# Optimization experiments

Hardware: AMD Instinct MI355X
Metric: run time of the kernel (lower is better)

## Reference

```python
import jax, jax.numpy as jnp
import numpy as np

# ---- constants from the source module ----
N_SAMPLES = 2 ** 15          # exp.n_samples
N_FRAMES = 128
N_HARMONICS = 8
N_EVENTS = 8
FILT_SIZE = 16               # freq_domain_filter_size
N_NOTES = 128                # len(scale)
NYQ = 22050.0 / 2.0          # samplerate nyquist
MIN_F0 = 40.0 / NYQ
F0_SPAN = (3000.0 / NYQ) - MIN_F0
MIN_RES = 0.5
RES_SPAN = 1.0 - MIN_RES
B_EVENTS = 128               # batch(16) * n_events(8)

# packed layout (build_param_slices order):
SL_F0 = slice(0, N_NOTES)                       # 0:128
SL_AMP = slice(N_NOTES + N_FRAMES, N_NOTES + 2 * N_FRAMES)   # 256:384
SL_HAMP = slice(N_NOTES + 2 * N_FRAMES, N_NOTES + 2 * N_FRAMES + N_HARMONICS)  # 384:392
SL_HDEC = slice(N_NOTES + 2 * N_FRAMES + N_HARMONICS, N_NOTES + 2 * N_FRAMES + 2 * N_HARMONICS)  # 392:400
SL_FENV = slice(N_NOTES + 2 * N_FRAMES + 2 * N_HARMONICS, N_NOTES + 2 * N_FRAMES + 2 * N_HARMONICS + FILT_SIZE)  # 400:416


def interp_linear(x, out_size):
    """F.interpolate(..., mode='linear', align_corners=False) on last dim of [B,C,L]."""
    L = x.shape[-1]
    scale = L / out_size
    coords = (jnp.arange(out_size, dtype=x.dtype) + 0.5) * scale - 0.5
    coords = jnp.clip(coords, 0.0, L - 1)
    i0 = jnp.floor(coords).astype(jnp.int32)
    i1 = jnp.minimum(i0 + 1, L - 1)
    w = coords - i0.astype(x.dtype)
    return x[..., i0] * (1.0 - w) + x[..., i1] * w


def setup_inputs() -> dict:
    key = jax.random.key(0)
    k1, k2 = jax.random.split(key)
    packed = jax.random.uniform(k1, (B_EVENTS, N_NOTES + 2 * N_FRAMES + 2 * N_HARMONICS + FILT_SIZE), dtype=jnp.float32)
    # musical-scale center frequencies, normalized by nyquist (geometric 20..3000 Hz)
    hz = 20.0 * (3000.0 / 20.0) ** (np.arange(N_NOTES) / (N_NOTES - 1))
    frequencies = jnp.asarray(hz / NYQ, dtype=jnp.float32)
    global_amp = jnp.full((1,), 5000.0, dtype=jnp.float32)
    osc_amp = jnp.full((1,), 50.0, dtype=jnp.float32)
    noise = jax.random.uniform(k2, (B_EVENTS, 1, N_SAMPLES), dtype=jnp.float32, minval=-1.0, maxval=1.0)
    return {"packed": packed, "frequencies": frequencies, "global_amp": global_amp,
            "osc_amp": osc_amp, "noise": noise}


def reference(packed, frequencies, global_amp, osc_amp, noise):
    B = packed.shape[0]
    # ---- f0 (discrete): softmax over notes, expectation, squared, repeated per frame ----
    f0_scalar = jax.nn.softmax(packed[:, SL_F0], axis=-1) @ frequencies          # [B]
    f0 = (f0_scalar ** 2)[:, None, None] * jnp.ones((1, 1, N_FRAMES), packed.dtype)  # [B,1,F]
    f0 = f0 * NYQ
    f0 = MIN_F0 + f0 * F0_SPAN
    # (the torch line `f0 + f0 + f0_fine` has no assignment -> no effect; f0_fine unused)

    # ---- oscillator bank ----
    harm_factors = jnp.arange(1, N_HARMONICS + 1, dtype=packed.dtype)
    osc = f0 * harm_factors[None, :, None]                      # [B,H,F]
    radians = osc / NYQ * jnp.pi
    radians = jnp.where(radians >= jnp.pi, 0.0, radians)
    radians = interp_linear(radians, N_SAMPLES)                  # [B,H,S]
    osc_bank = jnp.sin(jnp.cumsum(radians, axis=-1)) * osc_amp   # [B,H,S]

    # ---- per-harmonic amplitude recurrence (scan over frames) ----
    harm_decay = MIN_RES + packed[:, SL_HDEC] * RES_SPAN         # [B,H]
    harm_amp = packed[:, SL_HAMP]                                # [B,H]
    amp = packed[:, SL_AMP][:, None, :] * 2.0 - 1.0              # [B,1,F]

    def step(current, amp_i):                                    # current [B,H], amp_i [B,1]
        cur = jnp.maximum(current + amp_i * harm_amp, 0.0)       # clamp(0, inf)
        return cur * harm_decay, cur

    amp_frames = jnp.moveaxis(amp[:, 0, :], 1, 0)[:, :, None]    # [F,B,1]
    _, res = jax.lax.scan(step, jnp.zeros((B, N_HARMONICS), packed.dtype), amp_frames)
    res = jnp.moveaxis(res, 0, 2)                                # [B,H,F]
    res_full = interp_linear(res, N_SAMPLES)                     # [B,H,S]

    # ---- FFT-filtered noise ----
    amp_full = interp_linear(amp, N_SAMPLES)                     # [B,1,S]
    nf = packed[:, SL_FENV][:, None, :]                          # [B,1,16]
    nf = interp_linear(nf, N_SAMPLES // 2)
    nf = jnp.pad(nf, ((0, 0), (0, 0), (0, 1)))                   # [B,1,S//2+1]
    noise_scaled = noise * global_amp
    spec = jnp.fft.rfft(noise_scaled, axis=-1, norm='ortho')
    filt = spec * nf
    noise_out = jnp.fft.irfft(filt, n=N_SAMPLES, axis=-1, norm='ortho')
    noise_out = noise_out * jnp.where(amp_full >= 0, amp_full, 0.2 * amp_full)  # leaky_relu(0.2)

    # ---- combine ----
    x = res_full * osc_bank                                      # [B,H,S]
    x = noise_out / N_HARMONICS + x                              # broadcast [B,1,S]
    x = x.reshape(-1, N_EVENTS, N_HARMONICS, N_SAMPLES)
    x = jnp.sum(x, axis=(1, 2)).reshape(-1, 1, N_SAMPLES)        # [batch,1,S]
    return x
```

## Files before the change

### kernel.cpp

```cpp
#include <hip/hip_runtime.h>
#include <math.h>

#define PCK_STRIDE 416
#define N_SAMPLES  32768
#define FFT_M      16384
#define B_EVENTS   128
#define N_GROUPS   16
#define NT         1024
#define PI_F 3.14159265358979323846f
#define RT2H 0.70710678118654752f

#define MAP(i) ((i) + (((i) >> 5) << 2))
#define LDS_N  18432

__device__ inline float filt_at(const float* __restrict__ f, int k) {
    if (k >= FFT_M) return 0.0f;
    float c = ((float)k + 0.5f) * (1.0f / 1024.0f) - 0.5f;
    c = fminf(fmaxf(c, 0.0f), 15.0f);
    int i0 = (int)floorf(c);
    int i1 = min(i0 + 1, 15);
    float w = c - (float)i0;
    return f[i0] * (1.0f - w) + f[i1] * w;
}

template<int L>
__device__ inline void r4_dif_stage(float* re, float* im, int tid) {
    constexpr int q = L >> 2;
    constexpr float ang = -6.28318530717958647692f / (float)L;
    #pragma unroll 1
    for (int s = 0; s < (FFT_M / 4) / NT; ++s) {
        int m = tid + s * NT;
        int t = m & (q - 1);
        int i0 = ((m & ~(q - 1)) << 2) | t;
        int ia = MAP(i0), ib = MAP(i0 + q), ic = MAP(i0 + 2 * q), id = MAP(i0 + 3 * q);
        float ar = re[ia], ai = im[ia];
        float br = re[ib], bi = im[ib];
        float cr = re[ic], ci = im[ic];
        float dr = re[id], di = im[id];
        float s1, c1; __sincosf(ang * (float)t, &s1, &c1);
        float c2 = c1 * c1 - s1 * s1, s2 = 2.0f * c1 * s1;
        float c3 = c2 * c1 - s2 * s1, s3 = c2 * s1 + s2 * c1;
        float s0r = ar + cr, s0i = ai + ci;
        float t1r = br + dr, t1i = bi + di;
        float d0r = ar - cr, d0i = ai - ci;
        float d1r = br - dr, d1i = bi - di;
        re[ia] = s0r + t1r; im[ia] = s0i + t1i;
        float er = s0r - t1r, ei = s0i - t1i;
        re[ib] = er * c2 - ei * s2; im[ib] = er * s2 + ei * c2;
        float fr = d0r + d1i, fi = d0i - d1r;
        re[ic] = fr * c1 - fi * s1; im[ic] = fr * s1 + fi * c1;
        float gr = d0r - d1i, gi = d0i + d1r;
        re[id] = gr * c3 - gi * s3; im[id] = gr * s3 + gi * c3;
    }
    __syncthreads();
}

template<int L>
__device__ inline void r4_dit_stage(float* re, float* im, int tid) {
    constexpr int q = L >> 2;
    constexpr float ang = 6.28318530717958647692f / (float)L;
    #pragma unroll 1
    for (int s = 0; s < (FFT_M / 4) / NT; ++s) {
        int m = tid + s * NT;
        int t = m & (q - 1);
        int i0 = ((m & ~(q - 1)) << 2) | t;
        int ia = MAP(i0), ib = MAP(i0 + q), ic = MAP(i0 + 2 * q), id = MAP(i0 + 3 * q);
        float ar = re[ia], ai = im[ia];
        float br = re[ib], bi = im[ib];
        float cr = re[ic], ci = im[ic];
        float dr = re[id], di = im[id];
        float s1, c1; __sincosf(ang * (float)t, &s1, &c1);
        float c2 = c1 * c1 - s1 * s1, s2 = 2.0f * c1 * s1;
        float tbr = br * c2 - bi * s2, tbi = br * s2 + bi * c2;
        float tdr = dr * c2 - di * s2, tdi = dr * s2 + di * c2;
        float B0r = ar + tbr, B0i = ai + tbi;
        float B1r = ar - tbr, B1i = ai - tbi;
        float B2r = cr + tdr, B2i = ci + tdi;
        float B3r = cr - tdr, B3i = ci - tdi;
        float t0r = B2r * c1 - B2i * s1, t0i = B2r * s1 + B2i * c1;
        float t1r = -B3r * s1 - B3i * c1, t1i = B3r * c1 - B3i * s1;
        re[ia] = B0r + t0r; im[ia] = B0i + t0i;
        re[ib] = B1r + t1r; im[ib] = B1i + t1i;
        re[ic] = B0r - t0r; im[ic] = B0i - t0i;
        re[id] = B1r - t1r; im[id] = B1i - t1i;
    }
    __syncthreads();
}

__global__ __launch_bounds__(NT)
void fft_filter_kernel(
    const float* __restrict__ noise, const float* __restrict__ packed,
    const float* __restrict__ gamp, float* __restrict__ noise_out,
    const float* __restrict__ freqs, float* __restrict__ rW, float* __restrict__ res)
{
    extern __shared__ float smem[];
    float* re = smem;
    float* im = smem + LDS_N;
    float* filt = smem + 2 * LDS_N;
    const int b = blockIdx.x;
    const int tid = threadIdx.x;
    const float g = gamp[0];

    const float2* nz = (const float2*)(noise + (size_t)b * N_SAMPLES);
    #pragma unroll 1
    for (int s = 0; s < 8192 / NT; ++s) {
        int j = tid + s * NT;
        float2 v0 = nz[j];
        float2 v1 = nz[j + 8192];
        float ur = v0.x * g, ui = v0.y * g;
        float wr = v1.x * g, wi = v1.y * g;
        float s1, c1; __sincosf((-PI_F / 8192.0f) * (float)j, &s1, &c1);
        int a0 = MAP(j), a1 = MAP(j + 8192);
        re[a0] = ur + wr; im[a0] = ui + wi;
        float dr = ur - wr, di = ui - wi;
        re[a1] = dr * c1 - di * s1;
        im[a1] = dr * s1 + di * c1;
    }
    if (tid >= 64 && tid < 80) filt[tid - 64] = packed[b * PCK_STRIDE + 400 + (tid - 64)];

    if (tid < 64) {
        const float* row = packed + b * PCK_STRIDE;
        float n0 = row[tid], n1 = row[tid + 64];
        float fq0 = freqs[tid], fq1 = freqs[tid + 64];
        float mx = fmaxf(n0, n1);
        #pragma unroll
        for (int off = 32; off >= 1; off >>= 1) mx = fmaxf(mx, __shfl_xor(mx, off));
        float e0 = __expf(n0 - mx), e1 = __expf(n1 - mx);
        float den = e0 + e1, num = e0 * fq0 + e1 * fq1;
        #pragma unroll
        for (int off = 32; off >= 1; off >>= 1) {
            den += __shfl_xor(den, off);
            num += __shfl_xor(num, off);
        }
        float ampA = row[256 + tid] * 2.0f - 1.0f;
        float ampB = row[320 + tid] * 2.0f - 1.0f;
        int h = tid & 7;
        float ha = row[384 + h];
        float hd = 0.5f + row[392 + h] * 0.5f;
        const float MIN_F0 = 40.0f / 11025.0f;
        const float F0_SPAN = 3000.0f / 11025.0f - 40.0f / 11025.0f;
        float f0s = num / den;
        float f0 = MIN_F0 + f0s * f0s * 11025.0f * F0_SPAN;
        float r = f0 * (float)(h + 1) * (PI_F / 11025.0f);
        if (r >= PI_F) r = 0.0f;
        if (tid < 8) rW[b * 8 + tid] = r;
        float cur = 0.0f;
        float* rr = res + (b * 8 + h) * 128;
        for (int f = 0; f < 64; ++f) {
            float av = __shfl(ampA, f);
            float c = fmaxf(cur + av * ha, 0.0f);
            if (tid < 8) rr[f] = c;
            cur = c * hd;
        }
        for (int f = 0; f < 64; ++f) {
            float av = __shfl(ampB, f);
            float c = fmaxf(cur + av * ha, 0.0f);
            if (tid < 8) rr[64 + f] = c;
            cur = c * hd;
        }
    }
    __syncthreads();

    r4_dif_stage<8192>(re, im, tid);
    r4_dif_stage<2048>(re, im, tid);
    r4_dif_stage<512>(re, im, tid);
    r4_dif_stage<128>(re, im, tid);
    r4_dif_stage<32>(re, im, tid);

    #pragma unroll 1
    for (int s = 0; s < 2048 / NT; ++s) {
        int m = (2048 / NT) * tid + s;
        int a = MAP(8 * m);
        float4 r0 = *(const float4*)(re + a);
        float4 r1 = *(const float4*)(re + a + 4);
        float4 q0 = *(const float4*)(im + a);
        float4 q1 = *(const float4*)(im + a + 4);
        float t0r = r0.x + r1.x, t0i = q0.x + q1.x;
        float u0r = r0.x - r1.x, u0i = q0.x - q1.x;
        float d1r = r0.y - r1.y, d1i = q0.y - q1.y;
        float t1r = r0.y + r1.y, t1i = q0.y + q1.y;
        float u1r = RT2H * (d1r + d1i), u1i = RT2H * (d1i - d1r);
        float t2r = r0.z + r1.z, t2i = q0.z + q1.z;
        float d2r = r0.z - r1.z, d2i = q0.z - q1.z;
        float u2r = d2i, u2i = -d2r;
        float t3r = r0.w + r1.w, t3i = q0.w + q1.w;
        float d3r = r0.w - r1.w, d3i = q0.w - q1.w;
        float u3r = RT2H * (d3i - d3r), u3i = -RT2H * (d3r + d3i);
        float A0r = t0r + t2r, A0i = t0i + t2i;
        float A2r = t0r - t2r, A2i = t0i - t2i;
        float A1r = t1r + t3r, A1i = t1i + t3i;
        float e3r = t1r - t3r, e3i = t1i - t3i;
        float A3r = e3i, A3i = -e3r;
        float B0r = u0r + u2r, B0i = u0i + u2i;
        float B2r = u0r - u2r, B2i = u0i - u2i;
        float B1r = u1r + u3r, B1i = u1i + u3i;
        float f3r = u1r - u3r, f3i = u1i - u3i;
        float B3r = f3i, B3i = -f3r;
        r0.x = A0r + A1r; q0.x = A0i + A1i;
        r0.y = A0r - A1r; q0.y = A0i - A1i;
        r0.z = A2r + A3r; q0.z = A2i + A3i;
        r0.w = A2r - A3r; q0.w = A2i - A3i;
        r1.x = B0r + B1r; q1.x = B0i + B1i;
        r1.y = B0r - B1r; q1.y = B0i - B1i;
        r1.z = B2r + B3r; q1.z = B2i + B3i;
        r1.w = B2r - B3r; q1.w = B2i - B3i;
        *(float4*)(re + a) = r0; *(float4*)(re + a + 4) = r1;
        *(float4*)(im + a) = q0; *(float4*)(im + a + 4) = q1;
    }
    __syncthreads();

    const float invM = 1.0f / (float)FFT_M;
    #pragma unroll 1
    for (int s = 0; s < 8192 / NT; ++s) {
        int jj = (tid + s * NT) << 1;
        if (jj == 0) {
            int p0 = MAP(0);
            float z0r = re[p0], z0i = im[p0];
            float y = 0.5f * filt_at(filt, 0) * (z0r + z0i) * invM;
            re[p0] = y; im[p0] = y;
            int p1 = MAP(1);
            float H = filt_at(filt, 8192) * invM;
            re[p1] *= H; im[p1] *= H;
        } else {
            int k = (int)(__brev((unsigned)jj) >> 18);
            int kq = FFT_M - k;
            int pk = MAP(jj);
            int pq = MAP((int)(__brev((unsigned)kq) >> 18));
            float zkr = re[pk], zki = im[pk];
            float zqr = re[pq], zqi = im[pq];
            float Er = 0.5f * (zkr + zqr), Ei = 0.5f * (zki - zqi);
            float Or = 0.5f * (zki + zqi), Oi = 0.5f * (zqr - zkr);
            float th = (float)k * (PI_F / (float)FFT_M);
            float s1, c1; __sincosf(th, &s1, &c1);
            float ts = -s1;
            float tOr = c1 * Or - ts * Oi;
            float tOi = c1 * Oi + ts * Or;
            float Hk = filt_at(filt, k);
            float Hq = filt_at(filt, kq);
            float Ykr = Hk * (Er + tOr), Yki = Hk * (Ei + tOi);
            float Cr  = Hq * (Er - tOr), Ci  = Hq * (Ei - tOi);
            float Ar = 0.5f * (Ykr + Cr), Ai = 0.5f * (Yki + Ci);
            float Br = 0.5f * (Ykr - Cr), Bi = 0.5f * (Yki - Ci);
            re[pk] = (Ar + ts * Br - c1 * Bi) * invM;
            im[pk] = (Ai + c1 * Br + ts * Bi) * invM;
            re[pq] = (Ar + c1 * Bi - ts * Br) * invM;
            im[pq] = (-Ai + c1 * Br + ts * Bi) * invM;
        }
    }
    __syncthreads();

    #pragma unroll 1
    for (int s = 0; s < 2048 / NT; ++s) {
        int m = (2048 / NT) * tid + s;
        int a = MAP(8 * m);
        float4 r0 = *(const float4*)(re + a);
        float4 r1 = *(const float4*)(re + a + 4);
        float4 q0 = *(const float4*)(im + a);
        float4 q1 = *(const float4*)(im + a + 4);
        float A0r = r0.x + r0.y, A0i = q0.x + q0.y;
        float A1r = r0.x - r0.y, A1i = q0.x - q0.y;
        float A2r = r0.z + r0.w, A2i = q0.z + q0.w;
        float A3r = r0.z - r0.w, A3i = q0.z - q0.w;
        float B0r = r1.x + r1.y, B0i = q1.x + q1.y;
        float B1r = r1.x - r1.y, B1i = q1.x - q1.y;
        float B2r = r1.z + r1.w, B2i = q1.z + q1.w;
        float B3r = r1.z - r1.w, B3i = q1.z - q1.w;
        float t0r = A0r + A2r, t0i = A0i + A2i;
        float t2r = A0r - A2r, t2i = A0i - A2i;
        float w3r = -A3i, w3i = A3r;
        float t1r = A1r + w3r, t1i = A1i + w3i;
        float t3r = A1r - w3r, t3i = A1i - w3i;
        float u0r = B0r + B2r, u0i = B0i + B2i;
        float u2r = B0r - B2r, u2i = B0i - B2i;
        float x3r = -B3i, x3i = B3r;
        float u1r = B1r + x3r, u1i = B1i + x3i;
        float u3r = B1r - x3r, u3i = B1i - x3i;
        float w1r = RT2H * (u1r - u1i), w1i = RT2H * (u1r + u1i);
        float w2r = -u2i,               w2i = u2r;
        float w5r = RT2H * (-u3r - u3i), w5i = RT2H * (u3r - u3i);
        r0.x = t0r + u0r; q0.x = t0i + u0i;
        r1.x = t0r - u0r; q1.x = t0i - u0i;
        r0.y = t1r + w1r; q0.y = t1i + w1i;
        r1.y = t1r - w1r; q1.y = t1i - w1i;
        r0.z = t2r + w2r; q0.z = t2i + w2i;
        r1.z = t2r - w2r; q1.z = t2i - w2i;
        r0.w = t3r + w5r; q0.w = t3i + w5i;
        r1.w = t3r - w5r; q1.w = t3i - w5i;
        *(float4*)(re + a) = r0; *(float4*)(re + a + 4) = r1;
        *(float4*)(im + a) = q0; *(float4*)(im + a + 4) = q1;
    }
    __syncthreads();

    r4_dit_stage<32>(re, im, tid);
    r4_dit_stage<128>(re, im, tid);
    r4_dit_stage<512>(re, im, tid);
    r4_dit_stage<2048>(re, im, tid);
    r4_dit_stage<8192>(re, im, tid);

    float2* oz = (float2*)(noise_out + (size_t)b * N_SAMPLES);
    #pragma unroll 1
    for (int s = 0; s < 8192 / NT; ++s) {
        int j = tid + s * NT;
        int a0 = MAP(j), a1 = MAP(j + 8192);
        float ur = re[a0], ui = im[a0];
        float xr = re[a1], xi = im[a1];
        float s1, c1; __sincosf((PI_F / 8192.0f) * (float)j, &s1, &c1);
        float wr = xr * c1 - xi * s1, wi = xr * s1 + xi * c1;
        oz[j] = make_float2(ur + wr, ui + wi);
        oz[j + 8192] = make_float2(ur - wr, ui - wi);
    }
}

__global__ __launch_bounds__(256) void assemble_kernel(
    const float* __restrict__ packed, const float* __restrict__ rW,
    const float* __restrict__ res, const float* __restrict__ noise_out,
    const float* __restrict__ oamp, float* __restrict__ out)
{
    const int g = blockIdx.y;
    const int chunk = blockIdx.x;
    const int tid = threadIdx.x;
    const int n = chunk * 256 + tid;
    const int fb = chunk - 1;

    __shared__ float s_res[8][8][3];
    __shared__ float s_ampf[8][3];
    __shared__ float s_r[8][8];
    if (tid < 192) {
        int e = tid / 24, rem = tid % 24, h = rem / 3, j = rem % 3;
        int f = min(max(fb + j, 0), 127);
        s_res[e][h][j] = res[((g * 8 + e) * 8 + h) * 128 + f];
    }
    if (tid < 24) {
        int e = tid / 3, j = tid % 3;
        int f = min(max(fb + j, 0), 127);
        s_ampf[e][j] = packed[(g * 8 + e) * PCK_STRIDE + 256 + f] * 2.0f - 1.0f;
    }
    if (tid >= 192 && tid < 256) {
        int u = tid - 192;
        s_r[u / 8][u % 8] = rW[g * 64 + u];
    }
    __syncthreads();

    float coords = ((float)n + 0.5f) * (1.0f / 256.0f) - 0.5f;
    coords = fminf(fmaxf(coords, 0.0f), 127.0f);
    int i0 = (int)floorf(coords);
    float w = coords - (float)i0;
    int j0 = i0 - fb;
    float osc50 = oamp[0];
    float pn = (float)(n + 1);
    float wm = 1.0f - w;

    float acc = 0.0f;
    #pragma unroll
    for (int e = 0; e < 8; ++e) {
        int b = g * 8 + e;
        float nv = noise_out[(size_t)b * N_SAMPLES + n];
        float av = s_ampf[e][j0] * wm + s_ampf[e][j0 + 1] * w;
        float gate = (av >= 0.0f) ? av : 0.2f * av;
        acc += nv * gate;
        float sn, cn; __sincosf(pn * s_r[e][0], &sn, &cn);
        float c2 = 2.0f * cn;
        float shm1 = 0.0f, sh = sn;
        #pragma unroll
        for (int h = 0; h < 8; ++h) {
            float rsv = s_res[e][h][j0] * wm + s_res[e][h][j0 + 1] * w;
            float sv = (s_r[e][h] != 0.0f) ? sh : 0.0f;
            acc += rsv * osc50 * sv;
            float nx = c2 * sh - shm1;
            shm1 = sh; sh = nx;
        }
    }
    out[(size_t)g * N_SAMPLES + n] = acc;
}

extern "C" void kernel_launch(void* const* d_in, const int* in_sizes, int n_in,
                              void* d_out, int out_size, void* d_ws, size_t ws_size,
                              hipStream_t stream) {
    const float* packed = (const float*)d_in[0];
    const float* freqs  = (const float*)d_in[1];
    const float* gamp   = (const float*)d_in[2];
    const float* oamp   = (const float*)d_in[3];
    const float* noise  = (const float*)d_in[4];
    float* out = (float*)d_out;

    float* ws = (float*)d_ws;
    float* noise_out = ws;
    float* res = ws + (size_t)B_EVENTS * N_SAMPLES;
    float* rW  = res + B_EVENTS * 8 * 128;

    fft_filter_kernel<<<B_EVENTS, NT, (2 * LDS_N + 16) * sizeof(float), stream>>>(
        noise, packed, gamp, noise_out, freqs, rW, res);
    assemble_kernel<<<dim3(N_SAMPLES / 256, N_GROUPS), 256, 0, stream>>>(
        packed, rW, res, noise_out, oamp, out);
}
```

Baseline: 117.8 us.

## Fuse assembly into FFT kernel with atomic accumulation into output

Removes the separate assemble kernel and the global noise_out/res/rW round trip. After the inverse FFT, each block applies the amplitude gate, synthesizes the harmonic oscillator sum from LDS-resident resonance and amp tables, and atomically adds its per-sample contribution into the group output, which is zeroed with a memset first. Each thread now processes 16 contiguous samples with an incremental sin/cos rotation. This adds 8-way atomic contention per output element, uncoalesced strided atomics, and rotation-accumulated rounding error, and it leaves only 128 blocks to do all of the work.

```diff
diff --git a/kernel.cpp b/kernel.cpp
--- a/kernel.cpp
+++ b/kernel.cpp
@@ -5,13 +5,13 @@
 #define N_SAMPLES  32768
 #define FFT_M      16384
 #define B_EVENTS   128
-#define N_GROUPS   16
 #define NT         1024
 #define PI_F 3.14159265358979323846f
 #define RT2H 0.70710678118654752f
 
 #define MAP(i) ((i) + (((i) >> 5) << 2))
 #define LDS_N  18432
+#define LDS_TOTAL (2 * LDS_N + 16 + 1024 + 128 + 8)
 
 __device__ inline float filt_at(const float* __restrict__ f, int k) {
     if (k >= FFT_M) return 0.0f;
@@ -90,13 +90,16 @@
 __global__ __launch_bounds__(NT)
 void fft_filter_kernel(
     const float* __restrict__ noise, const float* __restrict__ packed,
-    const float* __restrict__ gamp, float* __restrict__ noise_out,
-    const float* __restrict__ freqs, float* __restrict__ rW, float* __restrict__ res)
+    const float* __restrict__ gamp, const float* __restrict__ oamp,
+    const float* __restrict__ freqs, float* __restrict__ out)
 {
     extern __shared__ float smem[];
     float* re = smem;
     float* im = smem + LDS_N;
-    float* filt = smem + 2 * LDS_N;
+    float* filt   = smem + 2 * LDS_N;
+    float* s_resd = filt + 16;
+    float* s_amp  = s_resd + 1024;
+    float* s_rw   = s_amp + 128;
     const int b = blockIdx.x;
     const int tid = threadIdx.x;
     const float g = gamp[0];
@@ -134,6 +137,8 @@
         }
         float ampA = row[256 + tid] * 2.0f - 1.0f;
         float ampB = row[320 + tid] * 2.0f - 1.0f;
+        s_amp[tid] = ampA;
+        s_amp[64 + tid] = ampB;
         int h = tid & 7;
         float ha = row[384 + h];
         float hd = 0.5f + row[392 + h] * 0.5f;
@@ -142,20 +147,23 @@
         float f0s = num / den;
         float f0 = MIN_F0 + f0s * f0s * 11025.0f * F0_SPAN;
         float r = f0 * (float)(h + 1) * (PI_F / 11025.0f);
-        if (r >= PI_F) r = 0.0f;
-        if (tid < 8) rW[b * 8 + tid] = r;
+        float m = 1.0f;
+        if (r >= PI_F) { r = 0.0f; m = 0.0f; }
+        float scale = m * oamp[0];
+        if (tid < 8) s_rw[tid] = r;
         float cur = 0.0f;
-        float* rr = res + (b * 8 + h) * 128;
+        #pragma unroll 1
         for (int f = 0; f < 64; ++f) {
             float av = __shfl(ampA, f);
             float c = fmaxf(cur + av * ha, 0.0f);
-            if (tid < 8) rr[f] = c;
+            if (tid < 8) s_resd[h * 128 + f] = c * scale;
             cur = c * hd;
         }
+        #pragma unroll 1
         for (int f = 0; f < 64; ++f) {
             float av = __shfl(ampB, f);
             float c = fmaxf(cur + av * ha, 0.0f);
-            if (tid < 8) rr[64 + f] = c;
+            if (tid < 8) s_resd[h * 128 + 64 + f] = c * scale;
             cur = c * hd;
         }
     }
@@ -297,80 +305,65 @@
     r4_dit_stage<2048>(re, im, tid);
     r4_dit_stage<8192>(re, im, tid);
 
-    float2* oz = (float2*)(noise_out + (size_t)b * N_SAMPLES);
-    #pragma unroll 1
-    for (int s = 0; s < 8192 / NT; ++s) {
-        int j = tid + s * NT;
-        int a0 = MAP(j), a1 = MAP(j + 8192);
-        float ur = re[a0], ui = im[a0];
-        float xr = re[a1], xi = im[a1];
-        float s1, c1; __sincosf((PI_F / 8192.0f) * (float)j, &s1, &c1);
-        float wr = xr * c1 - xi * s1, wi = xr * s1 + xi * c1;
-        oz[j] = make_float2(ur + wr, ui + wi);
-        oz[j + 8192] = make_float2(ur - wr, ui - wi);
-    }
-}
-
-__global__ __launch_bounds__(256) void assemble_kernel(
-    const float* __restrict__ packed, const float* __restrict__ rW,
-    const float* __restrict__ res, const float* __restrict__ noise_out,
-    const float* __restrict__ oamp, float* __restrict__ out)
-{
-    const int g = blockIdx.y;
-    const int chunk = blockIdx.x;
-    const int tid = threadIdx.x;
-    const int n = chunk * 256 + tid;
-    const int fb = chunk - 1;
-
-    __shared__ float s_res[8][8][3];
-    __shared__ float s_ampf[8][3];
-    __shared__ float s_r[8][8];
-    if (tid < 192) {
-        int e = tid / 24, rem = tid % 24, h = rem / 3, j = rem % 3;
-        int f = min(max(fb + j, 0), 127);
-        s_res[e][h][j] = res[((g * 8 + e) * 8 + h) * 128 + f];
-    }
-    if (tid < 24) {
-        int e = tid / 3, j = tid % 3;
-        int f = min(max(fb + j, 0), 127);
-        s_ampf[e][j] = packed[(g * 8 + e) * PCK_STRIDE + 256 + f] * 2.0f - 1.0f;
-    }
-    if (tid >= 192 && tid < 256) {
-        int u = tid - 192;
-        s_r[u / 8][u % 8] = rW[g * 64 + u];
-    }
-    __syncthreads();
-
-    float coords = ((float)n + 0.5f) * (1.0f / 256.0f) - 0.5f;
-    coords = fminf(fmaxf(coords, 0.0f), 127.0f);
-    int i0 = (int)floorf(coords);
-    float w = coords - (float)i0;
-    int j0 = i0 - fb;
-    float osc50 = oamp[0];
-    float pn = (float)(n + 1);
-    float wm = 1.0f - w;
-
-    float acc = 0.0f;
-    #pragma unroll
-    for (int e = 0; e < 8; ++e) {
-        int b = g * 8 + e;
-        float nv = noise_out[(size_t)b * N_SAMPLES + n];
-        float av = s_ampf[e][j0] * wm + s_ampf[e][j0 + 1] * w;
-        float gate = (av >= 0.0f) ? av : 0.2f * av;
-        acc += nv * gate;
-        float sn, cn; __sincosf(pn * s_r[e][0], &sn, &cn);
-        float c2 = 2.0f * cn;
-        float shm1 = 0.0f, sh = sn;
-        #pragma unroll
-        for (int h = 0; h < 8; ++h) {
-            float rsv = s_res[e][h][j0] * wm + s_res[e][h][j0 + 1] * w;
-            float sv = (s_r[e][h] != 0.0f) ? sh : 0.0f;
-            acc += rsv * osc50 * sv;
-            float nx = c2 * sh - shm1;
-            shm1 = sh; sh = nx;
-        }
-    }
-    out[(size_t)g * N_SAMPLES + n] = acc;
+    {
+        float* outg = out + (size_t)(b >> 3) * N_SAMPLES;
+        const float r1v = s_rw[0];
+        float rs, rc; __sincosf(r1v, &rs, &rc);
+        #pragma unroll 1
+        for (int run = 0; run < 2; ++run) {
+            const int tbase = 16 * tid + run * 16384;
+            float sn, cn; __sincosf((float)(tbase + 1) * r1v, &sn, &cn);
+            int cur = -1;
+            float Ah[8], Bh[8];
+            float aA = 0.0f, aB = 0.0f;
+            #pragma unroll 1
+            for (int s = 0; s < 8; ++s) {
+                const int j = 8 * tid + s;
+                const int a0 = MAP(j), a1 = MAP(j + 8192);
+                float ur = re[a0], ui = im[a0];
+                float xr = re[a1], xi = im[a1];
+                float s1, c1; __sincosf((PI_F / 8192.0f) * (float)j, &s1, &c1);
+                float wr = xr * c1 - xi * s1, wi = xr * s1 + xi * c1;
+                float vre = run ? (ur - wr) : (ur + wr);
+                float vim = run ? (ui - wi) : (ui + wi);
+                float vv0 = vre, vv1 = vim;
+                #pragma unroll
+                for (int ci = 0; ci < 2; ++ci) {
+                    const int n = tbase + 2 * s + ci;
+                    float coords = ((float)n + 0.5f) * (1.0f / 256.0f) - 0.5f;
+                    coords = fminf(fmaxf(coords, 0.0f), 127.0f);
+                    int i0 = (int)floorf(coords);
+                    float w = coords - (float)i0;
+                    if (i0 != cur) {
+                        cur = i0;
+                        int i1 = min(i0 + 1, 127);
+                        aA = s_amp[i0]; aB = s_amp[i1] - aA;
+                        #pragma unroll
+                        for (int h = 0; h < 8; ++h) {
+                            float a = s_resd[h * 128 + i0];
+                            Ah[h] = a;
+                            Bh[h] = s_resd[h * 128 + i1] - a;
+                        }
+                    }
+                    float av = aA + w * aB;
+                    float gate = (av >= 0.0f) ? av : 0.2f * av;
+                    float acc = (ci ? vv1 : vv0) * gate;
+                    float c2x = 2.0f * cn;
+                    float shm1 = 0.0f, sh = sn;
+                    #pragma unroll
+                    for (int h = 0; h < 8; ++h) {
+                        acc += (Ah[h] + w * Bh[h]) * sh;
+                        float nx = c2x * sh - shm1;
+                        shm1 = sh; sh = nx;
+                    }
+                    atomicAdd(&outg[n], acc);
+                    float ns = sn * rc + cn * rs;
+                    float nc = cn * rc - sn * rs;
+                    sn = ns; cn = nc;
+                }
+            }
+        }
+    }
 }
 
 extern "C" void kernel_launch(void* const* d_in, const int* in_sizes, int n_in,
@@ -383,13 +376,7 @@
     const float* noise  = (const float*)d_in[4];
     float* out = (float*)d_out;
 
-    float* ws = (float*)d_ws;
-    float* noise_out = ws;
-    float* res = ws + (size_t)B_EVENTS * N_SAMPLES;
-    float* rW  = res + B_EVENTS * 8 * 128;
-
-    fft_filter_kernel<<<B_EVENTS, NT, (2 * LDS_N + 16) * sizeof(float), stream>>>(
-        noise, packed, gamp, noise_out, freqs, rW, res);
-    assemble_kernel<<<dim3(N_SAMPLES / 256, N_GROUPS), 256, 0, stream>>>(
-        packed, rW, res, noise_out, oamp, out);
-}
+    hipMemsetAsync(out, 0, (size_t)out_size * sizeof(float), stream);
+    fft_filter_kernel<<<B_EVENTS, NT, LDS_TOTAL * sizeof(float), stream>>>(
+        noise, packed, gamp, oamp, freqs, out);
+}
```

After: 306.0 us. 2.6x slower.
